# Optimization experiments

Measured on AMD Instinct MI355X. Metric: run time of the kernel, lower is better.

## Reference

```python
import jax, jax.numpy as jnp
import numpy as np

B = 64  # batch_size (number of graphs)


def _leaky(v):
    return jax.nn.leaky_relu(v, 0.01)


def _gine(x, src, dst, edge_attr, ew, eb, w1, b1, w2, b2):
    # GINEConv (eps=0): out = nn(x + sum_{j->i} relu(x_j + lin(edge_attr)))
    n = x.shape[0]
    msg = jax.nn.relu(x[src] + edge_attr @ ew + eb)      # [E, C]
    agg = jax.ops.segment_sum(msg, dst, num_segments=n)  # [N, C]
    h = x + agg
    h = _leaky(h @ w1 + b1)
    h = _leaky(h @ w2 + b2)
    return h


def setup_inputs() -> dict:
    key = jax.random.key(0)
    ks = jax.random.split(key, 32)
    N, E, NF, EF, H, A = 65536, 1048576, 32, 16, 128, 10
    s = 0.05
    inp = {
        'x': jax.random.normal(ks[0], (N, NF), jnp.float32),
        'edge_index': jax.random.randint(ks[1], (2, E), 0, N, jnp.int64)
        if jax.config.jax_enable_x64 else jax.random.randint(ks[1], (2, E), 0, N, jnp.int32),
        'edge_attr': jax.random.normal(ks[2], (E, EF), jnp.float32),
        'e1_w': jax.random.normal(ks[3], (EF, NF)) * s, 'e1_b': jnp.zeros((NF,)),
        'c1_w1': jax.random.normal(ks[4], (NF, H)) * s, 'c1_b1': jnp.zeros((H,)),
        'c1_w2': jax.random.normal(ks[5], (H, H)) * s, 'c1_b2': jnp.zeros((H,)),
        'e2_w': jax.random.normal(ks[6], (EF, H)) * s, 'e2_b': jnp.zeros((H,)),
        'c2_w1': jax.random.normal(ks[7], (H, H)) * s, 'c2_b1': jnp.zeros((H,)),
        'c2_w2': jax.random.normal(ks[8], (H, H)) * s, 'c2_b2': jnp.zeros((H,)),
        'a_w1': jax.random.normal(ks[9], (H, H)) * s, 'a_b1': jnp.zeros((H,)),
        'a_w2': jax.random.normal(ks[10], (H, A)) * s, 'a_b2': jnp.zeros((A,)),
        'n_w1': jax.random.normal(ks[11], (H, H)) * s, 'n_b1': jnp.zeros((H,)),
        'n_w2': jax.random.normal(ks[12], (H, H)) * s, 'n_b2': jnp.zeros((H,)),
        'n_w3': jax.random.normal(ks[13], (H, 1)) * s, 'n_b3': jnp.zeros((1,)),
    }
    return inp


def reference(x, edge_index, edge_attr,
              e1_w, e1_b, c1_w1, c1_b1, c1_w2, c1_b2,
              e2_w, e2_b, c2_w1, c2_b1, c2_w2, c2_b2,
              a_w1, a_b1, a_w2, a_b2,
              n_w1, n_b1, n_w2, n_b2, n_w3, n_b3):
    src, dst = edge_index[0], edge_index[1]
    h = _gine(x, src, dst, edge_attr, e1_w, e1_b, c1_w1, c1_b1, c1_w2, c1_b2)
    h = jax.nn.relu(h)  # dropout is identity in eval mode
    h = _gine(h, src, dst, edge_attr, e2_w, e2_b, c2_w1, c2_b1, c2_w2, c2_b2)
    H = h.shape[-1]
    hb = h.reshape(B, -1, H)            # [B, Nper, H]
    pooled = hb.mean(axis=1)            # [B, H]
    a = _leaky(_leaky(pooled @ a_w1 + a_b1) @ a_w2 + a_b2)
    action_prob = jax.nn.softmax(a, axis=1)
    # reinterpret flat node order as [Nper, B, H], as in the torch reshape
    xr = h.reshape(-1, B, H)
    nh = _leaky(xr @ n_w1 + n_b1)
    nh = _leaky(nh @ n_w2 + n_b2)
    node_scores = jax.nn.sigmoid(nh @ n_w3 + n_b3)[..., 0].T  # [B, Nper]
    return action_prob, node_scores
```

## Files before the change

### kernel.cpp

```cpp
#include <hip/hip_runtime.h>
#include <math.h>

#define NNODES 65536
#define NEDGES 1048576
#define NF 32
#define EF 16
#define HD 128
#define NACT 10
#define NB 64
#define NPER 1024

typedef unsigned short u16;
typedef float  vf4  __attribute__((ext_vector_type(4)));
typedef __bf16 vbf8 __attribute__((ext_vector_type(8)));
#define BC8(v) __builtin_bit_cast(vbf8, v)

__device__ __forceinline__ float leakyf(float v) { return v > 0.0f ? v : 0.01f * v; }

__device__ __forceinline__ u16 f2bf(float x) {
    unsigned u = __float_as_uint(x);
    return (u16)((u + 0x7FFFu + ((u >> 16) & 1u)) >> 16);
}
__device__ __forceinline__ float bf2f(u16 h) { return __uint_as_float(((unsigned)h) << 16); }

__device__ __forceinline__ void cvt4(const float4 s, uint2& hi, uint2& lo) {
    const u16 h0 = f2bf(s.x), h1 = f2bf(s.y), h2 = f2bf(s.z), h3 = f2bf(s.w);
    hi = make_uint2((unsigned)h0 | ((unsigned)h1 << 16), (unsigned)h2 | ((unsigned)h3 << 16));
    const u16 l0 = f2bf(s.x - bf2f(h0)), l1 = f2bf(s.y - bf2f(h1));
    const u16 l2 = f2bf(s.z - bf2f(h2)), l3 = f2bf(s.w - bf2f(h3));
    lo = make_uint2((unsigned)l0 | ((unsigned)l1 << 16), (unsigned)l2 | ((unsigned)l3 << 16));
}

__global__ __launch_bounds__(256) void hist_kernel(const int* __restrict__ ei, int* __restrict__ cnt)
{
    const int i = blockIdx.x * 256 + threadIdx.x;
    if (i < NEDGES) atomicAdd(&cnt[ei[NEDGES + i]], 1);
}

__global__ __launch_bounds__(1024) void scan_kernel(const int* __restrict__ cnt, int* __restrict__ rs)
{
    __shared__ int s[1024];
    const int t = threadIdx.x;
    int loc[64];
    int tot = 0;
    const int4* c4 = (const int4*)(cnt + t * 64);
    #pragma unroll
    for (int j = 0; j < 16; ++j) {
        const int4 v = c4[j];
        loc[4*j+0] = v.x; loc[4*j+1] = v.y; loc[4*j+2] = v.z; loc[4*j+3] = v.w;
        tot += v.x + v.y + v.z + v.w;
    }
    s[t] = tot;
    __syncthreads();
    for (int off = 1; off < 1024; off <<= 1) {
        const int v = (t >= off) ? s[t - off] : 0;
        __syncthreads();
        s[t] += v;
        __syncthreads();
    }
    int run = s[t] - tot;
    #pragma unroll
    for (int j = 0; j < 64; ++j) { rs[t * 64 + j] = run; run += loc[j]; }
    if (t == 0) rs[NNODES] = NEDGES;
}

__global__ __launch_bounds__(256) void scatter_kernel(
    const int* __restrict__ ei, const int* __restrict__ rs, int* __restrict__ fill,
    int* __restrict__ ssrc, int* __restrict__ seidx)
{
    const int i = blockIdx.x * 256 + threadIdx.x;
    if (i < NEDGES) {
        const int d = ei[NEDGES + i];
        const int pos = rs[d] + atomicAdd(&fill[d], 1);
        ssrc[pos]  = ei[i];
        seidx[pos] = i;
    }
}

__global__ __launch_bounds__(256) void permute_kernel(
    const int* __restrict__ seidx, const float* __restrict__ ea, float* __restrict__ sea)
{
    const int t = blockIdx.x * 256 + threadIdx.x;
    const int e = t >> 2, part = t & 3;
    const int idx = seidx[e];
    ((float4*)sea)[(size_t)e * 4 + part] = ((const float4*)ea)[(size_t)idx * 4 + part];
}

__global__ __launch_bounds__(256) void pack_all_kernel(
    const float* __restrict__ w0, const float* __restrict__ w1, const float* __restrict__ w2,
    const float* __restrict__ w3, const float* __restrict__ w4, const float* __restrict__ w5,
    u16* __restrict__ pw)
{
    const int bid = blockIdx.x;
    const float* W; int KB, seg, sbase;
    if (bid < 16) { W = w0; KB = 1; seg = 0; sbase = 0; }
    else {
        const int i = (bid - 16) >> 6;
        seg = i + 1; sbase = 16 + i * 64; KB = 4;
        W = (i == 0) ? w1 : (i == 1) ? w2 : (i == 2) ? w3 : (i == 3) ? w4 : w5;
    }
    const int t = (bid - sbase) * 256 + threadIdx.x;
    const int j = t & 7, lane = (t >> 3) & 63, rest = t >> 9;
    const int kb = rest % KB, fb = rest / KB;
    if (fb >= 8) return;
    const int k = kb * 32 + (lane >> 4) * 8 + j;
    const int f = fb * 16 + (lane & 15);
    const float val = W[k * HD + f];
    const u16 h = f2bf(val);
    u16* dst = pw + seg * 32768;
    dst[t] = h;
    dst[16384 + t] = f2bf(val - bf2f(h));
}

__global__ __launch_bounds__(256) void e1_agg_kernel(
    const float* __restrict__ x, const int* __restrict__ rs,
    const int* __restrict__ ssrc, const float* __restrict__ sea,
    const float* __restrict__ w, const float* __restrict__ b, float* __restrict__ agg)
{
    const int tid  = threadIdx.x;
    const int lane = tid & 63;
    const int f    = lane & 31;
    const int half = lane >> 5;
    const int node = blockIdx.x * 4 + (tid >> 6);
    float wr[EF];
    #pragma unroll
    for (int k = 0; k < EF; ++k) wr[k] = w[k * NF + f];
    const float bf = b[f];
    const int beg = rs[node], end = rs[node + 1];
    float acc = 0.0f;
    int e = beg + half;
    for (; e + 2 < end; e += 4) {
        const int sA = ssrc[e], sB = ssrc[e + 2];
        const float4* pA = (const float4*)sea + (size_t)e * 4;
        const float4* pB = (const float4*)sea + (size_t)(e + 2) * 4;
        const float4 A0 = pA[0], A1 = pA[1], A2 = pA[2], A3 = pA[3];
        const float4 B0 = pB[0], B1 = pB[1], B2 = pB[2], B3 = pB[3];
        const float xA = x[(size_t)sA * NF + f];
        const float xB = x[(size_t)sB * NF + f];
        float evA[EF] = {A0.x,A0.y,A0.z,A0.w, A1.x,A1.y,A1.z,A1.w,
                         A2.x,A2.y,A2.z,A2.w, A3.x,A3.y,A3.z,A3.w};
        float evB[EF] = {B0.x,B0.y,B0.z,B0.w, B1.x,B1.y,B1.z,B1.w,
                         B2.x,B2.y,B2.z,B2.w, B3.x,B3.y,B3.z,B3.w};
        float mA = bf, mB = bf;
        #pragma unroll
        for (int k = 0; k < EF; ++k) {
            mA = fmaf(evA[k], wr[k], mA);
            mB = fmaf(evB[k], wr[k], mB);
        }
        acc += fmaxf(xA + mA, 0.0f) + fmaxf(xB + mB, 0.0f);
    }
    for (; e < end; e += 2) {
        const int sA = ssrc[e];
        const float4* pA = (const float4*)sea + (size_t)e * 4;
        const float4 A0 = pA[0], A1 = pA[1], A2 = pA[2], A3 = pA[3];
        float evA[EF] = {A0.x,A0.y,A0.z,A0.w, A1.x,A1.y,A1.z,A1.w,
                         A2.x,A2.y,A2.z,A2.w, A3.x,A3.y,A3.z,A3.w};
        float mA = bf;
        #pragma unroll
        for (int k = 0; k < EF; ++k) mA = fmaf(evA[k], wr[k], mA);
        acc += fmaxf(x[(size_t)sA * NF + f] + mA, 0.0f);
    }
    acc += __shfl_xor(acc, 32, 64);
    if (half == 0) agg[(size_t)node * NF + f] = acc;
}

__global__ __launch_bounds__(256) void e2_agg_kernel(
    const float* __restrict__ h, const int* __restrict__ rs,
    const int* __restrict__ ssrc, const float* __restrict__ sea,
    const float* __restrict__ w, const float* __restrict__ b, float* __restrict__ agg)
{
    const int tid  = threadIdx.x;
    const int lane = tid & 63;
    const int f    = lane * 2;
    const int node = blockIdx.x * 4 + (tid >> 6);
    float wr0[EF], wr1[EF];
    #pragma unroll
    for (int k = 0; k < EF; ++k) { wr0[k] = w[k * HD + f]; wr1[k] = w[k * HD + f + 1]; }
    const float b0 = b[f], b1 = b[f + 1];
    const int beg = __builtin_amdgcn_readfirstlane(rs[node]);
    const int end = __builtin_amdgcn_readfirstlane(rs[node + 1]);
    float acc0 = 0.0f, acc1 = 0.0f;
    int e = beg;
    for (; e + 2 <= end; e += 2) {
        const int sA = ssrc[e];
        const int sB = ssrc[e + 1];
        const float2 hA = *(const float2*)&h[(size_t)sA * HD + f];
        const float2 hB = *(const float2*)&h[(size_t)sB * HD + f];
        const float* aA = &sea[(size_t)e * EF];
        const float* aB = aA + EF;
        float mA0 = b0, mA1 = b1, mB0 = b0, mB1 = b1;
        #pragma unroll
        for (int k = 0; k < EF; ++k) {
            const float vA = aA[k];
            const float vB = aB[k];
            mA0 = fmaf(vA, wr0[k], mA0);
            mA1 = fmaf(vA, wr1[k], mA1);
            mB0 = fmaf(vB, wr0[k], mB0);
            mB1 = fmaf(vB, wr1[k], mB1);
        }
        acc0 += fmaxf(hA.x + mA0, 0.0f) + fmaxf(hB.x + mB0, 0.0f);
        acc1 += fmaxf(hA.y + mA1, 0.0f) + fmaxf(hB.y + mB1, 0.0f);
    }
    if (e < end) {
        const int sA = ssrc[e];
        const float2 hA = *(const float2*)&h[(size_t)sA * HD + f];
        const float* aA = &sea[(size_t)e * EF];
        float mA0 = b0, mA1 = b1;
        #pragma unroll
        for (int k = 0; k < EF; ++k) {
            const float vA = aA[k];
            mA0 = fmaf(vA, wr0[k], mA0);
            mA1 = fmaf(vA, wr1[k], mA1);
        }
        acc0 += fmaxf(hA.x + mA0, 0.0f);
        acc1 += fmaxf(hA.y + mA1, 0.0f);
    }
    *(float2*)&agg[(size_t)node * HD + f] = make_float2(acc0, acc1);
}

#define ROW128 272
#define ROW32  80

__device__ __forceinline__ void mfma_layer128(
    const unsigned char* __restrict__ aH, const unsigned char* __restrict__ aL,
    const u16* __restrict__ wH, const u16* __restrict__ wL,
    const float* __restrict__ bias, int lane, vf4* __restrict__ acc)
{
    const int quad = lane >> 4, fm = lane & 15;
    int4 Bh[4], Bl[4];
    #pragma unroll
    for (int kb = 0; kb < 4; ++kb) {
        Bh[kb] = *(const int4*)(aH + fm * ROW128 + kb * 64 + quad * 16);
        Bl[kb] = *(const int4*)(aL + fm * ROW128 + kb * 64 + quad * 16);
    }
    #pragma unroll
    for (int fb = 0; fb < 8; ++fb) {
        const float4 bv = *(const float4*)&bias[fb * 16 + quad * 4];
        vf4 a = {bv.x, bv.y, bv.z, bv.w};
        #pragma unroll
        for (int kb = 0; kb < 4; ++kb) {
            const int4 wh = *(const int4*)(wH + ((fb * 4 + kb) * 64 + lane) * 8);
            const int4 wl = *(const int4*)(wL + ((fb * 4 + kb) * 64 + lane) * 8);
            a = __builtin_amdgcn_mfma_f32_16x16x32_bf16(BC8(wh), BC8(Bl[kb]), a, 0, 0, 0);
            a = __builtin_amdgcn_mfma_f32_16x16x32_bf16(BC8(wl), BC8(Bh[kb]), a, 0, 0, 0);
            a = __builtin_amdgcn_mfma_f32_16x16x32_bf16(BC8(wh), BC8(Bh[kb]), a, 0, 0, 0);
        }
        acc[fb] = a;
    }
}

__device__ __forceinline__ void mfma_layer32(
    const unsigned char* __restrict__ aH, const unsigned char* __restrict__ aL,
    const u16* __restrict__ wH, const u16* __restrict__ wL,
    const float* __restrict__ bias, int lane, vf4* __restrict__ acc)
{
    const int quad = lane >> 4, fm = lane & 15;
    const int4 Bh = *(const int4*)(aH + fm * ROW32 + quad * 16);
    const int4 Bl = *(const int4*)(aL + fm * ROW32 + quad * 16);
    #pragma unroll
    for (int fb = 0; fb < 8; ++fb) {
        const float4 bv = *(const float4*)&bias[fb * 16 + quad * 4];
        vf4 a = {bv.x, bv.y, bv.z, bv.w};
        const int4 wh = *(const int4*)(wH + (fb * 64 + lane) * 8);
        const int4 wl = *(const int4*)(wL + (fb * 64 + lane) * 8);
        a = __builtin_amdgcn_mfma_f32_16x16x32_bf16(BC8(wh), BC8(Bl), a, 0, 0, 0);
        a = __builtin_amdgcn_mfma_f32_16x16x32_bf16(BC8(wl), BC8(Bh), a, 0, 0, 0);
        a = __builtin_amdgcn_mfma_f32_16x16x32_bf16(BC8(wh), BC8(Bh), a, 0, 0, 0);
        acc[fb] = a;
    }
}

__device__ __forceinline__ void store_act_leaky(
    unsigned char* __restrict__ aH, unsigned char* __restrict__ aL, int lane, vf4* __restrict__ acc)
{
    const int quad = lane >> 4, fm = lane & 15;
    #pragma unroll
    for (int fb = 0; fb < 8; ++fb) {
        const float4 s = {leakyf(acc[fb][0]), leakyf(acc[fb][1]), leakyf(acc[fb][2]), leakyf(acc[fb][3])};
        acc[fb][0] = s.x; acc[fb][1] = s.y; acc[fb][2] = s.z; acc[fb][3] = s.w;
        uint2 phi, plo;
        cvt4(s, phi, plo);
        *(uint2*)(aH + fm * ROW128 + fb * 32 + quad * 8) = phi;
        *(uint2*)(aL + fm * ROW128 + fb * 32 + quad * 8) = plo;
    }
}

__global__ __launch_bounds__(256) void n1_kernel(
    const float* __restrict__ x, const float* __restrict__ agg,
    const u16* __restrict__ w1h, const u16* __restrict__ w1l, const float* __restrict__ b1,
    const u16* __restrict__ w2h, const u16* __restrict__ w2l, const float* __restrict__ b2,
    float* __restrict__ hout)
{
    __shared__ __align__(16) unsigned char smem[4][2560 + 2 * 16 * ROW128];
    const int tid = threadIdx.x, lane = tid & 63, wid = tid >> 6;
    const int quad = lane >> 4, fm = lane & 15;
    const int tile = blockIdx.x * 4 + wid;
    unsigned char* inH = smem[wid];
    unsigned char* inL = inH + 16 * ROW32;
    unsigned char* aH  = inH + 2560;
    unsigned char* aL  = aH + 16 * ROW128;
    const size_t base = (size_t)tile * 16 * NF;
    #pragma unroll
    for (int i = 0; i < 2; ++i) {
        const int flat = i * 64 + lane;
        const int node = flat >> 3, kq = flat & 7;
        const float4 xv = *(const float4*)&x[base + node * NF + kq * 4];
        const float4 av = *(const float4*)&agg[base + node * NF + kq * 4];
        const float4 s = {xv.x + av.x, xv.y + av.y, xv.z + av.z, xv.w + av.w};
        uint2 phi, plo;
        cvt4(s, phi, plo);
        *(uint2*)(inH + node * ROW32 + kq * 8) = phi;
        *(uint2*)(inL + node * ROW32 + kq * 8) = plo;
    }
    __syncthreads();
    vf4 acc[8];
    mfma_layer32(inH, inL, w1h, w1l, b1, lane, acc);
    __syncthreads();
    store_act_leaky(aH, aL, lane, acc);
    __syncthreads();
    mfma_layer128(aH, aL, w2h, w2l, b2, lane, acc);
    const size_t ob = (size_t)tile * 16 * HD;
    #pragma unroll
    for (int fb = 0; fb < 8; ++fb) {
        const float4 o = {fmaxf(acc[fb][0], 0.0f), fmaxf(acc[fb][1], 0.0f),
                          fmaxf(acc[fb][2], 0.0f), fmaxf(acc[fb][3], 0.0f)};
        *(float4*)&hout[ob + fm * HD + fb * 16 + quad * 4] = o;
    }
}

__global__ __launch_bounds__(256) void n2_kernel(
    const float* __restrict__ h, const float* __restrict__ agg,
    const u16* __restrict__ w1h, const u16* __restrict__ w1l, const float* __restrict__ b1,
    const u16* __restrict__ w2h, const u16* __restrict__ w2l, const float* __restrict__ b2,
    const u16* __restrict__ m1h, const u16* __restrict__ m1l, const float* __restrict__ nb1,
    const u16* __restrict__ m2h, const u16* __restrict__ m2l, const float* __restrict__ nb2,
    const float* __restrict__ nw3, const float* __restrict__ nb3,
    float* __restrict__ pooled, float* __restrict__ scores)
{
    __shared__ __align__(16) unsigned char smem[4][2 * 16 * ROW128];
    const int tid = threadIdx.x, lane = tid & 63, wid = tid >> 6;
    const int quad = lane >> 4, fm = lane & 15;
    const int tile = blockIdx.x * 4 + wid;
    unsigned char* aH = smem[wid];
    unsigned char* aL = aH + 16 * ROW128;
    const size_t base = (size_t)tile * 16 * HD;
    #pragma unroll
    for (int i = 0; i < 8; ++i) {
        const int flat = i * 64 + lane;
        const int node = flat >> 5, kq = flat & 31;
        const float4 hv = *(const float4*)&h[base + node * HD + kq * 4];
        const float4 av = *(const float4*)&agg[base + node * HD + kq * 4];
        const float4 s = {hv.x + av.x, hv.y + av.y, hv.z + av.z, hv.w + av.w};
        uint2 phi, plo;
        cvt4(s, phi, plo);
        *(uint2*)(aH + node * ROW128 + kq * 8) = phi;
        *(uint2*)(aL + node * ROW128 + kq * 8) = plo;
    }
    __syncthreads();
    vf4 acc[8];
    mfma_layer128(aH, aL, w1h, w1l, b1, lane, acc);
    __syncthreads();
    store_act_leaky(aH, aL, lane, acc);
    __syncthreads();
    mfma_layer128(aH, aL, w2h, w2l, b2, lane, acc);
    __syncthreads();
    store_act_leaky(aH, aL, lane, acc);
    {
        const int g = tile >> 6;
        #pragma unroll
        for (int fb = 0; fb < 8; ++fb) {
            vf4 t = acc[fb];
            #pragma unroll
            for (int off = 1; off < 16; off <<= 1) {
                t[0] += __shfl_xor(t[0], off, 64);
                t[1] += __shfl_xor(t[1], off, 64);
                t[2] += __shfl_xor(t[2], off, 64);
                t[3] += __shfl_xor(t[3], off, 64);
            }
            #pragma unroll
            for (int r = 0; r < 4; ++r) {
                const int item = fb * 4 + r;
                if (fm == (item >> 1))
                    atomicAdd(&pooled[g * HD + fb * 16 + quad * 4 + r], t[r]);
            }
        }
    }
    __syncthreads();
    mfma_layer128(aH, aL, m1h, m1l, nb1, lane, acc);
    __syncthreads();
    store_act_leaky(aH, aL, lane, acc);
    __syncthreads();
    mfma_layer128(aH, aL, m2h, m2l, nb2, lane, acc);
    float v = 0.0f;
    #pragma unroll
    for (int fb = 0; fb < 8; ++fb) {
        const float4 w3v = *(const float4*)&nw3[fb * 16 + quad * 4];
        v += leakyf(acc[fb][0]) * w3v.x + leakyf(acc[fb][1]) * w3v.y
           + leakyf(acc[fb][2]) * w3v.z + leakyf(acc[fb][3]) * w3v.w;
    }
    v += __shfl_xor(v, 16, 64);
    v += __shfl_xor(v, 32, 64);
    if (lane < 16) {
        const int node = tile * 16 + fm;
        const float s = v + nb3[0];
        scores[(node & 63) * NPER + (node >> 6)] = 1.0f / (1.0f + expf(-s));
    }
}

__global__ __launch_bounds__(128) void act_kernel(
    const float* __restrict__ pooled,
    const float* __restrict__ w1, const float* __restrict__ b1,
    const float* __restrict__ w2, const float* __restrict__ b2,
    float* __restrict__ out)
{
    __shared__ __align__(16) float p[HD];
    __shared__ float a1[HD];
    __shared__ float z[NACT];
    __shared__ float red2[2];
    const int g = blockIdx.x;
    const int tid = threadIdx.x;
    p[tid] = pooled[g * HD + tid] * (1.0f / NPER);
    __syncthreads();
    float acc = b1[tid];
    for (int k = 0; k < HD; ++k) acc = fmaf(p[k], w1[k * HD + tid], acc);
    a1[tid] = leakyf(acc);
    __syncthreads();
    if (tid < NACT) {
        float a2 = b2[tid];
        for (int k = 0; k < HD; ++k) a2 = fmaf(a1[k], w2[k * NACT + tid], a2);
        z[tid] = leakyf(a2);
    }
    __syncthreads();
    if (tid == 0) {
        float m = z[0];
        for (int i = 1; i < NACT; ++i) m = fmaxf(m, z[i]);
        red2[0] = m;
    }
    __syncthreads();
    if (tid < NACT) z[tid] = expf(z[tid] - red2[0]);
    __syncthreads();
    if (tid == 0) {
        float s = 0.0f;
        for (int i = 0; i < NACT; ++i) s += z[i];
        red2[1] = s;
    }
    __syncthreads();
    if (tid < NACT) out[g * NACT + tid] = z[tid] / red2[1];
}

extern "C" void kernel_launch(void* const* d_in, const int* in_sizes, int n_in,
                              void* d_out, int out_size, void* d_ws, size_t ws_size,
                              hipStream_t stream)
{
    const float* x    = (const float*)d_in[0];
    const int*   ei   = (const int*)d_in[1];
    const float* ea   = (const float*)d_in[2];
    const float* e1w  = (const float*)d_in[3];
    const float* e1b  = (const float*)d_in[4];
    const float* c1w1 = (const float*)d_in[5];
    const float* c1b1 = (const float*)d_in[6];
    const float* c1w2 = (const float*)d_in[7];
    const float* c1b2 = (const float*)d_in[8];
    const float* e2w  = (const float*)d_in[9];
    const float* e2b  = (const float*)d_in[10];
    const float* c2w1 = (const float*)d_in[11];
    const float* c2b1 = (const float*)d_in[12];
    const float* c2w2 = (const float*)d_in[13];
    const float* c2b2 = (const float*)d_in[14];
    const float* aw1  = (const float*)d_in[15];
    const float* ab1  = (const float*)d_in[16];
    const float* aw2  = (const float*)d_in[17];
    const float* ab2  = (const float*)d_in[18];
    const float* nw1  = (const float*)d_in[19];
    const float* nb1  = (const float*)d_in[20];
    const float* nw2  = (const float*)d_in[21];
    const float* nb2  = (const float*)d_in[22];
    const float* nw3  = (const float*)d_in[23];
    const float* nb3  = (const float*)d_in[24];

    float* out = (float*)d_out;
    char*  ws  = (char*)d_ws;
    const size_t MB = 1024 * 1024;
    float* h      = (float*)(ws);
    float* agg2   = (float*)(ws + 32  * MB);
    int*   seidx  = (int*)  (ws + 32  * MB);
    float* sea    = (float*)(ws + 64  * MB);
    float* agg1   = (float*)(ws + 128 * MB);
    float* pooled = (float*)(ws + 136 * MB);
    u16*   pw     = (u16*)  (ws + 136 * MB + 64 * 1024);
    int*   cnt    = (int*)  (ws + 137 * MB);
    int*   fill   = (int*)  (ws + 137 * MB + 256 * 1024);
    int*   rs     = (int*)  (ws + 139 * MB);
    int*   ssrc   = (int*)  (ws + 140 * MB);

    u16* p_c1w1 = pw;
    u16* p_c1w2 = pw + 1 * 32768;
    u16* p_c2w1 = pw + 2 * 32768;
    u16* p_c2w2 = pw + 3 * 32768;
    u16* p_nw1  = pw + 4 * 32768;
    u16* p_nw2  = pw + 5 * 32768;

    hipMemsetAsync(cnt,    0, 2 * NNODES * sizeof(int), stream);
    hipMemsetAsync(pooled, 0, (size_t)NB * HD * sizeof(float), stream);

    pack_all_kernel<<<336, 256, 0, stream>>>(c1w1, c1w2, c2w1, c2w2, nw1, nw2, pw);

    hist_kernel<<<NEDGES / 256, 256, 0, stream>>>(ei, cnt);
    scan_kernel<<<1, 1024, 0, stream>>>(cnt, rs);
    scatter_kernel<<<NEDGES / 256, 256, 0, stream>>>(ei, rs, fill, ssrc, seidx);
    permute_kernel<<<NEDGES / 64, 256, 0, stream>>>(seidx, ea, sea);

    e1_agg_kernel<<<NNODES / 4, 256, 0, stream>>>(x, rs, ssrc, sea, e1w, e1b, agg1);
    n1_kernel<<<NNODES / 64, 256, 0, stream>>>(x, agg1,
                                               p_c1w1, p_c1w1 + 16384, c1b1,
                                               p_c1w2, p_c1w2 + 16384, c1b2, h);
    e2_agg_kernel<<<NNODES / 4, 256, 0, stream>>>(h, rs, ssrc, sea, e2w, e2b, agg2);
    n2_kernel<<<NNODES / 64, 256, 0, stream>>>(h, agg2,
                                               p_c2w1, p_c2w1 + 16384, c2b1,
                                               p_c2w2, p_c2w2 + 16384, c2b2,
                                               p_nw1,  p_nw1  + 16384, nb1,
                                               p_nw2,  p_nw2  + 16384, nb2,
                                               nw3, nb3, pooled, out + NB * NACT);
    act_kernel<<<NB, 128, 0, stream>>>(pooled, aw1, ab1, aw2, ab2, out);
}
```

Baseline: 581.8 us.

## Drop low-bf16 activation split in hidden MLP layers and pack edge FMAs

```diff
diff --git a/kernel.cpp b/kernel.cpp
--- a/kernel.cpp
+++ b/kernel.cpp
@@ -11,11 +11,15 @@
 #define NPER 1024
 
 typedef unsigned short u16;
+typedef float  vf2  __attribute__((ext_vector_type(2)));
 typedef float  vf4  __attribute__((ext_vector_type(4)));
 typedef __bf16 vbf8 __attribute__((ext_vector_type(8)));
 #define BC8(v) __builtin_bit_cast(vbf8, v)
 
 __device__ __forceinline__ float leakyf(float v) { return v > 0.0f ? v : 0.01f * v; }
+__device__ __forceinline__ vf2 fma2(vf2 a, vf2 b, vf2 c) { return __builtin_elementwise_fma(a, b, c); }
+__device__ __forceinline__ vf2 max2(vf2 a, vf2 b) { return __builtin_elementwise_max(a, b); }
+__device__ __forceinline__ vf2 splat2(float s) { vf2 r = {s, s}; return r; }
 
 __device__ __forceinline__ u16 f2bf(float x) {
     unsigned u = __float_as_uint(x);
@@ -29,6 +33,10 @@
     const u16 l0 = f2bf(s.x - bf2f(h0)), l1 = f2bf(s.y - bf2f(h1));
     const u16 l2 = f2bf(s.z - bf2f(h2)), l3 = f2bf(s.w - bf2f(h3));
     lo = make_uint2((unsigned)l0 | ((unsigned)l1 << 16), (unsigned)l2 | ((unsigned)l3 << 16));
+}
+__device__ __forceinline__ uint2 cvt4hi(const float4 s) {
+    const u16 h0 = f2bf(s.x), h1 = f2bf(s.y), h2 = f2bf(s.z), h3 = f2bf(s.w);
+    return make_uint2((unsigned)h0 | ((unsigned)h1 << 16), (unsigned)h2 | ((unsigned)h3 << 16));
 }
 
 __global__ __launch_bounds__(256) void hist_kernel(const int* __restrict__ ei, int* __restrict__ cnt)
@@ -119,49 +127,34 @@
 {
     const int tid  = threadIdx.x;
     const int lane = tid & 63;
-    const int f    = lane & 31;
-    const int half = lane >> 5;
+    const int p    = lane & 15;
+    const int q    = lane >> 4;
     const int node = blockIdx.x * 4 + (tid >> 6);
-    float wr[EF];
-    #pragma unroll
-    for (int k = 0; k < EF; ++k) wr[k] = w[k * NF + f];
-    const float bf = b[f];
+    vf2 wr[EF];
+    #pragma unroll
+    for (int k = 0; k < EF; ++k) wr[k] = *(const vf2*)&w[k * NF + p * 2];
+    const vf2 bias = *(const vf2*)&b[p * 2];
     const int beg = rs[node], end = rs[node + 1];
-    float acc = 0.0f;
-    int e = beg + half;
-    for (; e + 2 < end; e += 4) {
-        const int sA = ssrc[e], sB = ssrc[e + 2];
-        const float4* pA = (const float4*)sea + (size_t)e * 4;
-        const float4* pB = (const float4*)sea + (size_t)(e + 2) * 4;
-        const float4 A0 = pA[0], A1 = pA[1], A2 = pA[2], A3 = pA[3];
-        const float4 B0 = pB[0], B1 = pB[1], B2 = pB[2], B3 = pB[3];
-        const float xA = x[(size_t)sA * NF + f];
-        const float xB = x[(size_t)sB * NF + f];
-        float evA[EF] = {A0.x,A0.y,A0.z,A0.w, A1.x,A1.y,A1.z,A1.w,
-                         A2.x,A2.y,A2.z,A2.w, A3.x,A3.y,A3.z,A3.w};
-        float evB[EF] = {B0.x,B0.y,B0.z,B0.w, B1.x,B1.y,B1.z,B1.w,
-                         B2.x,B2.y,B2.z,B2.w, B3.x,B3.y,B3.z,B3.w};
-        float mA = bf, mB = bf;
-        #pragma unroll
-        for (int k = 0; k < EF; ++k) {
-            mA = fmaf(evA[k], wr[k], mA);
-            mB = fmaf(evB[k], wr[k], mB);
-        }
-        acc += fmaxf(xA + mA, 0.0f) + fmaxf(xB + mB, 0.0f);
-    }
-    for (; e < end; e += 2) {
+    vf2 acc = {0.0f, 0.0f};
+    for (int e = beg + q; e < end; e += 4) {
         const int sA = ssrc[e];
         const float4* pA = (const float4*)sea + (size_t)e * 4;
         const float4 A0 = pA[0], A1 = pA[1], A2 = pA[2], A3 = pA[3];
-        float evA[EF] = {A0.x,A0.y,A0.z,A0.w, A1.x,A1.y,A1.z,A1.w,
-                         A2.x,A2.y,A2.z,A2.w, A3.x,A3.y,A3.z,A3.w};
-        float mA = bf;
-        #pragma unroll
-        for (int k = 0; k < EF; ++k) mA = fmaf(evA[k], wr[k], mA);
-        acc += fmaxf(x[(size_t)sA * NF + f] + mA, 0.0f);
-    }
-    acc += __shfl_xor(acc, 32, 64);
-    if (half == 0) agg[(size_t)node * NF + f] = acc;
+        const vf2 xv = *(const vf2*)((const char*)x + (((unsigned)sA << 7) + (unsigned)p * 8));
+        vf2 m = bias;
+        m = fma2(splat2(A0.x), wr[0],  m); m = fma2(splat2(A0.y), wr[1],  m);
+        m = fma2(splat2(A0.z), wr[2],  m); m = fma2(splat2(A0.w), wr[3],  m);
+        m = fma2(splat2(A1.x), wr[4],  m); m = fma2(splat2(A1.y), wr[5],  m);
+        m = fma2(splat2(A1.z), wr[6],  m); m = fma2(splat2(A1.w), wr[7],  m);
+        m = fma2(splat2(A2.x), wr[8],  m); m = fma2(splat2(A2.y), wr[9],  m);
+        m = fma2(splat2(A2.z), wr[10], m); m = fma2(splat2(A2.w), wr[11], m);
+        m = fma2(splat2(A3.x), wr[12], m); m = fma2(splat2(A3.y), wr[13], m);
+        m = fma2(splat2(A3.z), wr[14], m); m = fma2(splat2(A3.w), wr[15], m);
+        acc += max2(xv + m, splat2(0.0f));
+    }
+    acc[0] += __shfl_xor(acc[0], 16, 64); acc[1] += __shfl_xor(acc[1], 16, 64);
+    acc[0] += __shfl_xor(acc[0], 32, 64); acc[1] += __shfl_xor(acc[1], 32, 64);
+    if (lane < 16) *(vf2*)&agg[(size_t)node * NF + p * 2] = acc;
 }
 
 __global__ __launch_bounds__(256) void e2_agg_kernel(
@@ -171,57 +164,48 @@
 {
     const int tid  = threadIdx.x;
     const int lane = tid & 63;
-    const int f    = lane * 2;
+    const unsigned foff = (unsigned)lane * 8;
     const int node = blockIdx.x * 4 + (tid >> 6);
-    float wr0[EF], wr1[EF];
-    #pragma unroll
-    for (int k = 0; k < EF; ++k) { wr0[k] = w[k * HD + f]; wr1[k] = w[k * HD + f + 1]; }
-    const float b0 = b[f], b1 = b[f + 1];
+    vf2 wr[EF];
+    #pragma unroll
+    for (int k = 0; k < EF; ++k) wr[k] = *(const vf2*)&w[k * HD + lane * 2];
+    const vf2 bias = *(const vf2*)&b[lane * 2];
     const int beg = __builtin_amdgcn_readfirstlane(rs[node]);
     const int end = __builtin_amdgcn_readfirstlane(rs[node + 1]);
-    float acc0 = 0.0f, acc1 = 0.0f;
+    vf2 acc = {0.0f, 0.0f};
     int e = beg;
     for (; e + 2 <= end; e += 2) {
         const int sA = ssrc[e];
         const int sB = ssrc[e + 1];
-        const float2 hA = *(const float2*)&h[(size_t)sA * HD + f];
-        const float2 hB = *(const float2*)&h[(size_t)sB * HD + f];
+        const vf2 hA = *(const vf2*)((const char*)h + (((unsigned)sA << 9) + foff));
+        const vf2 hB = *(const vf2*)((const char*)h + (((unsigned)sB << 9) + foff));
         const float* aA = &sea[(size_t)e * EF];
         const float* aB = aA + EF;
-        float mA0 = b0, mA1 = b1, mB0 = b0, mB1 = b1;
+        vf2 mA = bias, mB = bias;
         #pragma unroll
         for (int k = 0; k < EF; ++k) {
-            const float vA = aA[k];
-            const float vB = aB[k];
-            mA0 = fmaf(vA, wr0[k], mA0);
-            mA1 = fmaf(vA, wr1[k], mA1);
-            mB0 = fmaf(vB, wr0[k], mB0);
-            mB1 = fmaf(vB, wr1[k], mB1);
+            mA = fma2(splat2(aA[k]), wr[k], mA);
+            mB = fma2(splat2(aB[k]), wr[k], mB);
         }
-        acc0 += fmaxf(hA.x + mA0, 0.0f) + fmaxf(hB.x + mB0, 0.0f);
-        acc1 += fmaxf(hA.y + mA1, 0.0f) + fmaxf(hB.y + mB1, 0.0f);
+        acc += max2(hA + mA, splat2(0.0f));
+        acc += max2(hB + mB, splat2(0.0f));
     }
     if (e < end) {
         const int sA = ssrc[e];
-        const float2 hA = *(const float2*)&h[(size_t)sA * HD + f];
+        const vf2 hA = *(const vf2*)((const char*)h + (((unsigned)sA << 9) + foff));
         const float* aA = &sea[(size_t)e * EF];
-        float mA0 = b0, mA1 = b1;
+        vf2 mA = bias;
         #pragma unroll
-        for (int k = 0; k < EF; ++k) {
-            const float vA = aA[k];
-            mA0 = fmaf(vA, wr0[k], mA0);
-            mA1 = fmaf(vA, wr1[k], mA1);
-        }
-        acc0 += fmaxf(hA.x + mA0, 0.0f);
-        acc1 += fmaxf(hA.y + mA1, 0.0f);
-    }
-    *(float2*)&agg[(size_t)node * HD + f] = make_float2(acc0, acc1);
+        for (int k = 0; k < EF; ++k) mA = fma2(splat2(aA[k]), wr[k], mA);
+        acc += max2(hA + mA, splat2(0.0f));
+    }
+    *(vf2*)&agg[(size_t)node * HD + lane * 2] = acc;
 }
 
 #define ROW128 272
 #define ROW32  80
 
-__device__ __forceinline__ void mfma_layer128(
+__device__ __forceinline__ void mfma_layer128_in(
     const unsigned char* __restrict__ aH, const unsigned char* __restrict__ aL,
     const u16* __restrict__ wH, const u16* __restrict__ wL,
     const float* __restrict__ bias, int lane, vf4* __restrict__ acc)
@@ -249,7 +233,32 @@
     }
 }
 
-__device__ __forceinline__ void mfma_layer32(
+__device__ __forceinline__ void mfma_layer128_act(
+    const unsigned char* __restrict__ aH,
+    const u16* __restrict__ wH, const u16* __restrict__ wL,
+    const float* __restrict__ bias, int lane, vf4* __restrict__ acc)
+{
+    const int quad = lane >> 4, fm = lane & 15;
+    int4 Bh[4];
+    #pragma unroll
+    for (int kb = 0; kb < 4; ++kb)
+        Bh[kb] = *(const int4*)(aH + fm * ROW128 + kb * 64 + quad * 16);
+    #pragma unroll
+    for (int fb = 0; fb < 8; ++fb) {
+        const float4 bv = *(const float4*)&bias[fb * 16 + quad * 4];
+        vf4 a = {bv.x, bv.y, bv.z, bv.w};
+        #pragma unroll
+        for (int kb = 0; kb < 4; ++kb) {
+            const int4 wh = *(const int4*)(wH + ((fb * 4 + kb) * 64 + lane) * 8);
+            const int4 wl = *(const int4*)(wL + ((fb * 4 + kb) * 64 + lane) * 8);
+            a = __builtin_amdgcn_mfma_f32_16x16x32_bf16(BC8(wl), BC8(Bh[kb]), a, 0, 0, 0);
+            a = __builtin_amdgcn_mfma_f32_16x16x32_bf16(BC8(wh), BC8(Bh[kb]), a, 0, 0, 0);
+        }
+        acc[fb] = a;
+    }
+}
+
+__device__ __forceinline__ void mfma_layer32_in(
     const unsigned char* __restrict__ aH, const unsigned char* __restrict__ aL,
     const u16* __restrict__ wH, const u16* __restrict__ wL,
     const float* __restrict__ bias, int lane, vf4* __restrict__ acc)
@@ -270,18 +279,15 @@
     }
 }
 
-__device__ __forceinline__ void store_act_leaky(
-    unsigned char* __restrict__ aH, unsigned char* __restrict__ aL, int lane, vf4* __restrict__ acc)
+__device__ __forceinline__ void store_act_hi(
+    unsigned char* __restrict__ aH, int lane, vf4* __restrict__ acc)
 {
     const int quad = lane >> 4, fm = lane & 15;
     #pragma unroll
     for (int fb = 0; fb < 8; ++fb) {
         const float4 s = {leakyf(acc[fb][0]), leakyf(acc[fb][1]), leakyf(acc[fb][2]), leakyf(acc[fb][3])};
         acc[fb][0] = s.x; acc[fb][1] = s.y; acc[fb][2] = s.z; acc[fb][3] = s.w;
-        uint2 phi, plo;
-        cvt4(s, phi, plo);
-        *(uint2*)(aH + fm * ROW128 + fb * 32 + quad * 8) = phi;
-        *(uint2*)(aL + fm * ROW128 + fb * 32 + quad * 8) = plo;
+        *(uint2*)(aH + fm * ROW128 + fb * 32 + quad * 8) = cvt4hi(s);
     }
 }
 
@@ -291,14 +297,13 @@
     const u16* __restrict__ w2h, const u16* __restrict__ w2l, const float* __restrict__ b2,
     float* __restrict__ hout)
 {
-    __shared__ __align__(16) unsigned char smem[4][2560 + 2 * 16 * ROW128];
+    __shared__ __align__(16) unsigned char smem[4][2560 + 16 * ROW128];
     const int tid = threadIdx.x, lane = tid & 63, wid = tid >> 6;
     const int quad = lane >> 4, fm = lane & 15;
     const int tile = blockIdx.x * 4 + wid;
     unsigned char* inH = smem[wid];
     unsigned char* inL = inH + 16 * ROW32;
     unsigned char* aH  = inH + 2560;
-    unsigned char* aL  = aH + 16 * ROW128;
     const size_t base = (size_t)tile * 16 * NF;
     #pragma unroll
     for (int i = 0; i < 2; ++i) {
@@ -314,11 +319,11 @@
     }
     __syncthreads();
     vf4 acc[8];
-    mfma_layer32(inH, inL, w1h, w1l, b1, lane, acc);
-    __syncthreads();
-    store_act_leaky(aH, aL, lane, acc);
-    __syncthreads();
-    mfma_layer128(aH, aL, w2h, w2l, b2, lane, acc);
+    mfma_layer32_in(inH, inL, w1h, w1l, b1, lane, acc);
+    __syncthreads();
+    store_act_hi(aH, lane, acc);
+    __syncthreads();
+    mfma_layer128_act(aH, w2h, w2l, b2, lane, acc);
     const size_t ob = (size_t)tile * 16 * HD;
     #pragma unroll
     for (int fb = 0; fb < 8; ++fb) {
@@ -358,13 +363,13 @@
     }
     __syncthreads();
     vf4 acc[8];
-    mfma_layer128(aH, aL, w1h, w1l, b1, lane, acc);
-    __syncthreads();
-    store_act_leaky(aH, aL, lane, acc);
-    __syncthreads();
-    mfma_layer128(aH, aL, w2h, w2l, b2, lane, acc);
-    __syncthreads();
-    store_act_leaky(aH, aL, lane, acc);
+    mfma_layer128_in(aH, aL, w1h, w1l, b1, lane, acc);
+    __syncthreads();
+    store_act_hi(aH, lane, acc);
+    __syncthreads();
+    mfma_layer128_act(aH, w2h, w2l, b2, lane, acc);
+    __syncthreads();
+    store_act_hi(aH, lane, acc);
     {
         const int g = tile >> 6;
         #pragma unroll
@@ -386,11 +391,11 @@
         }
     }
     __syncthreads();
-    mfma_layer128(aH, aL, m1h, m1l, nb1, lane, acc);
-    __syncthreads();
-    store_act_leaky(aH, aL, lane, acc);
-    __syncthreads();
-    mfma_layer128(aH, aL, m2h, m2l, nb2, lane, acc);
+    mfma_layer128_act(aH, m1h, m1l, nb1, lane, acc);
+    __syncthreads();
+    store_act_hi(aH, lane, acc);
+    __syncthreads();
+    mfma_layer128_act(aH, m2h, m2l, nb2, lane, acc);
     float v = 0.0f;
     #pragma unroll
     for (int fb = 0; fb < 8; ++fb) {
```

Result: no change. 579.8 us (-0.3%).
